# Optimization experiments

Measured on AMD Instinct MI355X. Metric: run time of the kernel, lower is better.

The kernel has to match this reference:

```python
import jax, jax.numpy as jnp
import numpy as np

HEADS = 12
IDX = 0


def setup_inputs() -> dict:
    key = jax.random.key(0)
    ks = jax.random.split(key, 6)
    B, H, W, C = 16, 64, 64, 384
    x = jax.random.normal(ks[0], (B, H * W, C), dtype=jnp.float32)
    qkv_w = jax.random.normal(ks[1], (3 * C, C), dtype=jnp.float32) * 0.02
    proj_w = jax.random.normal(ks[2], (C, C), dtype=jnp.float32) * 0.02
    proj_b = jax.random.normal(ks[3], (C,), dtype=jnp.float32) * 0.02
    lepe_w = jax.random.normal(ks[4], (C, 1, 3, 3), dtype=jnp.float32) * 0.02  # depthwise, torch OIHW with I=1
    lepe_b = jax.random.normal(ks[5], (C,), dtype=jnp.float32) * 0.02
    return {"x": x, "qkv_w": qkv_w, "proj_w": proj_w, "proj_b": proj_b,
            "lepe_w": lepe_w, "lepe_b": lepe_b, "H": H, "W": W}


def _lepe_forward(x, qkv_w, proj_w, proj_b, lepe_w, lepe_b, H, W):
    B, N, C = x.shape
    hd = C // HEADS
    scale = hd ** (-0.5)
    x_img = x.reshape(B, H, W, C)

    if IDX == 0:
        # vertical strips: attend over H within each column
        x_split = jnp.transpose(x_img, (0, 2, 1, 3)).reshape(B * W, H, C)
    else:
        x_split = x_img.reshape(B * H, W, C)
    S, L, _ = x_split.shape

    qkv = (x_split @ qkv_w.T).reshape(S, L, 3, HEADS, hd)
    qkv = jnp.transpose(qkv, (2, 0, 3, 1, 4))  # (3, S, heads, L, hd)
    q, k, v = qkv[0], qkv[1], qkv[2]

    attn = jnp.einsum('shld,shmd->shlm', q, k) * scale
    attn = jax.nn.softmax(attn, axis=-1)
    out = jnp.einsum('shlm,shmd->shld', attn, v)           # (S, heads, L, hd)
    out = jnp.transpose(out, (0, 2, 1, 3)).reshape(S, L, C)
    # faithful to torch: view(B, out_H, out_W, C).view(B, H*W, C) -- no permute back for idx==0
    out_flat = out.reshape(B, H * W, C)

    # depthwise 3x3 conv LePE on the original (H, W) layout
    lepe = jax.lax.conv_general_dilated(
        jnp.transpose(x_img, (0, 3, 1, 2)), lepe_w,
        window_strides=(1, 1), padding='SAME',
        feature_group_count=C,
        dimension_numbers=('NCHW', 'OIHW', 'NCHW'))
    lepe = lepe + lepe_b[None, :, None, None]
    lepe = jnp.transpose(lepe, (0, 2, 3, 1)).reshape(B, H * W, C)

    return (out_flat + lepe) @ proj_w.T + proj_b


def reference(x, qkv_w, proj_w, proj_b, lepe_w, lepe_b, H, W):
    return _lepe_forward(x, qkv_w, proj_w, proj_b, lepe_w, lepe_b, H, W)
```

## Files before the change

### kernel.cpp

```cpp
#include <hip/hip_runtime.h>


typedef _Float16 f16;
typedef _Float16 f16x8 __attribute__((ext_vector_type(8)));
typedef float    f32x4 __attribute__((ext_vector_type(4)));

__device__ __forceinline__ f32x4 mfma_16x16x32(f16x8 a, f16x8 b, f32x4 c) {
  return __builtin_amdgcn_mfma_f32_16x16x32_f16(a, b, c, 0, 0, 0);
}

__global__ __launch_bounds__(256) void k_cvt(const float* __restrict__ src,
                                             f16* __restrict__ dst, int n8) {
  int i = blockIdx.x * 256 + threadIdx.x;
  if (i >= n8) return;
  const f32x4* s4 = (const f32x4*)src;
  f32x4 a = s4[2 * i], b = s4[2 * i + 1];
  f16x8 o;
#pragma unroll
  for (int j = 0; j < 4; ++j) { o[j] = (f16)a[j]; o[4 + j] = (f16)b[j]; }
  *(f16x8*)&dst[(long)i * 8] = o;
}

template <int NDIM, bool FINAL>
__global__ __launch_bounds__(256) void k_gemm(const f16* __restrict__ A,
                                              const f16* __restrict__ Bt,
                                              const float* __restrict__ bias,
                                              f16* __restrict__ Ch,
                                              float* __restrict__ Cf) {
  constexpr int KD = 384;
  constexpr int LDSP = 72;
  constexpr int NT = NDIM / 128;
  __shared__ f16 As[128 * LDSP];
  __shared__ f16 Bs[128 * LDSP];

  const int tid = threadIdx.x;
  const int lane = tid & 63;
  const int wave = tid >> 6;
  const int wr = wave >> 1, wc = wave & 1;
  const int ln = lane & 15, quad = lane >> 4;
  const int q8 = quad * 8;
  const int mt = blockIdx.x / NT;
  const int nt = blockIdx.x % NT;
  const long m0 = (long)mt * 128;
  const int n0 = nt * 128;

  f32x4 acc[4][4] = {};

  for (int k0 = 0; k0 < KD; k0 += 64) {
#pragma unroll
    for (int r = 0; r < 4; ++r) {
      int flat = r * 256 + tid;
      int row = flat >> 3;
      int kk = (flat & 7) * 8;
      f16x8 av = *(const f16x8*)&A[(m0 + row) * KD + k0 + kk];
      *(f16x8*)&As[row * LDSP + kk] = av;
      f16x8 bv = *(const f16x8*)&Bt[(long)(n0 + row) * KD + k0 + kk];
      *(f16x8*)&Bs[row * LDSP + kk] = bv;
    }
    __syncthreads();
#pragma unroll
    for (int ks = 0; ks < 2; ++ks) {
      f16x8 a[4], b[4];
#pragma unroll
      for (int i = 0; i < 4; ++i)
        a[i] = *(const f16x8*)&As[(wr * 64 + i * 16 + ln) * LDSP + ks * 32 + q8];
#pragma unroll
      for (int j = 0; j < 4; ++j)
        b[j] = *(const f16x8*)&Bs[(wc * 64 + j * 16 + ln) * LDSP + ks * 32 + q8];
#pragma unroll
      for (int i = 0; i < 4; ++i)
#pragma unroll
        for (int j = 0; j < 4; ++j)
          acc[i][j] = mfma_16x16x32(a[i], b[j], acc[i][j]);
    }
    __syncthreads();
  }

#pragma unroll
  for (int i = 0; i < 4; ++i) {
#pragma unroll
    for (int j = 0; j < 4; ++j) {
      int gc = n0 + wc * 64 + j * 16 + ln;
#pragma unroll
      for (int r = 0; r < 4; ++r) {
        long gr = m0 + wr * 64 + i * 16 + quad * 4 + r;
        float v = acc[i][j][r];
        if (FINAL)
          Cf[gr * NDIM + gc] = v + bias[gc];
        else
          Ch[gr * (long)NDIM + gc] = (f16)v;
      }
    }
  }
}

__global__ __launch_bounds__(256) void k_lepe(const f16* __restrict__ x16,
                                              const float* __restrict__ lw,
                                              const float* __restrict__ lb,
                                              f16* __restrict__ afused) {
  __shared__ float ws[384 * 9];
  __shared__ float bs[384];
  for (int i = threadIdx.x; i < 384 * 9; i += 256) ws[i] = lw[i];
  for (int i = threadIdx.x; i < 384; i += 256) bs[i] = lb[i];
  __syncthreads();

  int chunk = blockIdx.x * 256 + threadIdx.x;
  int token = chunk / 48;
  int c0 = (chunk % 48) * 8;
  int b = token >> 12, n = token & 4095;
  int h = n >> 6, w = n & 63;

  float acc[8];
#pragma unroll
  for (int cc = 0; cc < 8; ++cc) acc[cc] = bs[c0 + cc];
#pragma unroll
  for (int ky = 0; ky < 3; ++ky) {
    int hh = h + ky - 1;
    if (hh < 0 || hh > 63) continue;
#pragma unroll
    for (int kx = 0; kx < 3; ++kx) {
      int ww = w + kx - 1;
      if (ww < 0 || ww > 63) continue;
      f16x8 xv = *(const f16x8*)&x16[((long)((b << 12) + (hh << 6) + ww)) * 384 + c0];
#pragma unroll
      for (int cc = 0; cc < 8; ++cc)
        acc[cc] += (float)xv[cc] * ws[(c0 + cc) * 9 + ky * 3 + kx];
    }
  }
  f16x8 o;
#pragma unroll
  for (int cc = 0; cc < 8; ++cc) o[cc] = (f16)acc[cc];
  *(f16x8*)&afused[(long)token * 384 + c0] = o;
}

__global__ __launch_bounds__(64) void k_attn(const f16* __restrict__ qkv,
                                             f16* __restrict__ afused) {
  __shared__ f16 vt[32 * 72];
  __shared__ f16 qkbuf[2 * 64 * 56];
  f16* qs = qkbuf;
  f16* ks = qkbuf + 64 * 56;
  f16* ps = qkbuf;

  const int lane = threadIdx.x;
  const int hh = blockIdx.x % 12;
  const int s = blockIdx.x / 12;
  const int b = s >> 6, w = s & 63;
  const int ln = lane & 15, quad = lane >> 4;
  const int q8 = quad * 8;
  const long baseTok = ((long)b << 12) + w;

#pragma unroll
  for (int r = 0; r < 4; ++r) {
    int flat = r * 64 + lane;
    int l = flat >> 2;
    int dg = (flat & 3) * 8;
    long ta = (baseTok + (long)l * 64) * 1152 + hh * 32 + dg;
    f16x8 qv = *(const f16x8*)&qkv[ta];
    f16x8 kv = *(const f16x8*)&qkv[ta + 384];
    f16x8 vv = *(const f16x8*)&qkv[ta + 768];
    *(f16x8*)&qs[l * 56 + dg] = qv;
    *(f16x8*)&ks[l * 56 + dg] = kv;
#pragma unroll
    for (int ii = 0; ii < 8; ++ii) vt[(dg + ii) * 72 + l] = vv[ii];
  }
  __syncthreads();

  f16x8 aq[4], bk[4];
#pragma unroll
  for (int i = 0; i < 4; ++i) aq[i] = *(const f16x8*)&qs[(i * 16 + ln) * 56 + q8];
#pragma unroll
  for (int j = 0; j < 4; ++j) bk[j] = *(const f16x8*)&ks[(j * 16 + ln) * 56 + q8];
  f32x4 sc[4][4] = {};
#pragma unroll
  for (int i = 0; i < 4; ++i)
#pragma unroll
    for (int j = 0; j < 4; ++j) sc[i][j] = mfma_16x16x32(aq[i], bk[j], sc[i][j]);
  __syncthreads();

  const float scale = 0.17677669529663687f;
  float rs[4][4];
#pragma unroll
  for (int i = 0; i < 4; ++i) {
#pragma unroll
    for (int r = 0; r < 4; ++r) {
      float m = -1e30f;
#pragma unroll
      for (int j = 0; j < 4; ++j) m = fmaxf(m, sc[i][j][r]);
#pragma unroll
      for (int off = 1; off < 16; off <<= 1) m = fmaxf(m, __shfl_xor(m, off, 64));
      m *= scale;
      float sum = 0.f;
#pragma unroll
      for (int j = 0; j < 4; ++j) {
        float p = __expf(sc[i][j][r] * scale - m);
        sc[i][j][r] = p;
        sum += p;
      }
#pragma unroll
      for (int off = 1; off < 16; off <<= 1) sum += __shfl_xor(sum, off, 64);
      rs[i][r] = 1.0f / sum;
    }
  }

#pragma unroll
  for (int i = 0; i < 4; ++i)
#pragma unroll
    for (int j = 0; j < 4; ++j)
#pragma unroll
      for (int r = 0; r < 4; ++r)
        ps[(i * 16 + quad * 4 + r) * 72 + j * 16 + ln] = (f16)sc[i][j][r];
  __syncthreads();

  f32x4 oc[4][2] = {};
#pragma unroll
  for (int ks2 = 0; ks2 < 2; ++ks2) {
    f16x8 ap[4], bv[2];
#pragma unroll
    for (int i = 0; i < 4; ++i)
      ap[i] = *(const f16x8*)&ps[(i * 16 + ln) * 72 + ks2 * 32 + q8];
#pragma unroll
    for (int j = 0; j < 2; ++j)
      bv[j] = *(const f16x8*)&vt[(j * 16 + ln) * 72 + ks2 * 32 + q8];
#pragma unroll
    for (int i = 0; i < 4; ++i)
#pragma unroll
      for (int j = 0; j < 2; ++j) oc[i][j] = mfma_16x16x32(ap[i], bv[j], oc[i][j]);
  }

#pragma unroll
  for (int i = 0; i < 4; ++i)
#pragma unroll
    for (int j = 0; j < 2; ++j)
#pragma unroll
      for (int r = 0; r < 4; ++r) {
        int l = i * 16 + quad * 4 + r;
        int d = j * 16 + ln;
        long g = ((long)b * 4096 + w * 64 + l) * 384 + hh * 32 + d;
        float v = oc[i][j][r] * rs[i][r];
        afused[g] = (f16)(v + (float)afused[g]);
      }
}

extern "C" void kernel_launch(void* const* d_in, const int* in_sizes, int n_in,
                              void* d_out, int out_size, void* d_ws, size_t ws_size,
                              hipStream_t stream) {
  const float* x      = (const float*)d_in[0];
  const float* qkv_w  = (const float*)d_in[1];
  const float* proj_w = (const float*)d_in[2];
  const float* proj_b = (const float*)d_in[3];
  const float* lepe_w = (const float*)d_in[4];
  const float* lepe_b = (const float*)d_in[5];
  float* out = (float*)d_out;

  char* ws = (char*)d_ws;
  f16* x16    = (f16*)(ws + 0);
  f16* w16    = (f16*)(ws + 50331648);
  f16* pw16   = (f16*)(ws + 51216384);
  f16* qkv16  = (f16*)(ws + 51511296);
  f16* afused = (f16*)(ws + 202506240);

  k_cvt<<<12288, 256, 0, stream>>>(x, x16, 3145728);
  k_cvt<<<216, 256, 0, stream>>>(qkv_w, w16, 55296);
  k_cvt<<<72, 256, 0, stream>>>(proj_w, pw16, 18432);
  k_gemm<1152, false><<<512 * 9, 256, 0, stream>>>(x16, w16, nullptr, qkv16, nullptr);
  k_lepe<<<12288, 256, 0, stream>>>(x16, lepe_w, lepe_b, afused);
  k_attn<<<1024 * 12, 64, 0, stream>>>(qkv16, afused);
  k_gemm<384, true><<<512 * 3, 256, 0, stream>>>(afused, pw16, proj_b, nullptr, out);
}
```

Baseline: 508.0 us.

## Fuse LePE conv, QKV projection and strip attention into one kernel

Replaces the x fp16 conversion, the QKV GEMM, the LePE depthwise conv and the attention kernels with a single per-(batch, column) kernel. It computes LePE directly from fp32 x, builds per-head Q/K/V in LDS from register-held x fragments and weights read from global memory, then runs softmax attention and accumulates into afused. This removes the large qkv16 and x16 intermediates from HBM traffic and three launches. In exchange, every block rereads the full QKV weight matrix from cache, the grid drops to 1024 blocks, and there is a stray no-op multiply-by-zero term in the LePE loop.

```diff
diff --git a/kernel.cpp b/kernel.cpp
--- a/kernel.cpp
+++ b/kernel.cpp
@@ -3,6 +3,7 @@
 
 typedef _Float16 f16;
 typedef _Float16 f16x8 __attribute__((ext_vector_type(8)));
+typedef _Float16 f16x4 __attribute__((ext_vector_type(4)));
 typedef float    f32x4 __attribute__((ext_vector_type(4)));
 
 __device__ __forceinline__ f32x4 mfma_16x16x32(f16x8 a, f16x8 b, f32x4 c) {
@@ -19,6 +20,221 @@
 #pragma unroll
   for (int j = 0; j < 4; ++j) { o[j] = (f16)a[j]; o[4 + j] = (f16)b[j]; }
   *(f16x8*)&dst[(long)i * 8] = o;
+}
+
+__global__ __launch_bounds__(256, 2) void k_fused(const float* __restrict__ x,
+                                                  const f16* __restrict__ w16,
+                                                  const float* __restrict__ lw,
+                                                  const float* __restrict__ lb,
+                                                  f16* __restrict__ afused) {
+  __shared__ f16 shp[2][14592];
+  const int tid = threadIdx.x;
+  const int lane = tid & 63;
+  const int wave = tid >> 6;
+  const int mh = wave & 1, nh = wave >> 1;
+  const int ln = lane & 15, quad = lane >> 4, q8 = quad * 8;
+  const int b = blockIdx.x >> 6, w = blockIdx.x & 63;
+
+  f16* qs = shp[nh];
+  f16* ks = shp[nh] + 2560;
+  f16* vt = shp[nh] + 5120;
+  f16* ps = shp[nh] + 7424;
+  f16* obuf = shp[nh] + 12032;
+
+  {
+    const float* xb = x + (long)b * 4096 * 384;
+    const int l = lane;
+    f16* arow = afused + ((long)(b * 4096 + w * 64 + l)) * 384;
+#pragma unroll
+    for (int it = 0; it < 12; ++it) {
+      int c0 = (it * 4 + wave) * 8;
+      float a8[8];
+#pragma unroll
+      for (int cc = 0; cc < 8; ++cc) a8[cc] = lb[c0 + cc];
+#pragma unroll
+      for (int ky = 0; ky < 3; ++ky) {
+        int hh2 = w + ky - 1;
+        if (hh2 < 0 || hh2 > 63) continue;
+#pragma unroll
+        for (int kx = 0; kx < 3; ++kx) {
+          int ww2 = l + kx - 1;
+          if (ww2 < 0 || ww2 > 63) continue;
+          const float* p = xb + ((hh2 << 6) + ww2) * 384 + c0;
+          float4 u = *(const float4*)p;
+          float4 v2 = *(const float4*)(p + 4);
+#pragma unroll
+          for (int cc = 0; cc < 4; ++cc) {
+            a8[cc] += u.x * 0.f;
+          }
+#pragma unroll
+          for (int cc = 0; cc < 4; ++cc) {
+            float wv0 = lw[(c0 + cc) * 9 + ky * 3 + kx];
+            float wv1 = lw[(c0 + 4 + cc) * 9 + ky * 3 + kx];
+            float xv0 = (cc == 0) ? u.x : (cc == 1) ? u.y : (cc == 2) ? u.z : u.w;
+            float xv1 = (cc == 0) ? v2.x : (cc == 1) ? v2.y : (cc == 2) ? v2.z : v2.w;
+            a8[cc] += xv0 * wv0;
+            a8[4 + cc] += xv1 * wv1;
+          }
+        }
+      }
+      f16x8 o;
+#pragma unroll
+      for (int cc = 0; cc < 8; ++cc) o[cc] = (f16)a8[cc];
+      *(f16x8*)&arow[c0] = o;
+    }
+  }
+  __syncthreads();
+
+  f16x8 afr[12][2];
+  {
+    const float* xcol = x + ((long)(b * 4096) + w) * 384;
+#pragma unroll
+    for (int s = 0; s < 12; ++s)
+#pragma unroll
+      for (int i = 0; i < 2; ++i) {
+        const float* p = xcol + (long)(mh * 32 + i * 16 + ln) * 24576 + s * 32 + q8;
+        float4 u = *(const float4*)p;
+        float4 v2 = *(const float4*)(p + 4);
+        f16x8 t;
+        t[0] = (f16)u.x; t[1] = (f16)u.y; t[2] = (f16)u.z; t[3] = (f16)u.w;
+        t[4] = (f16)v2.x; t[5] = (f16)v2.y; t[6] = (f16)v2.z; t[7] = (f16)v2.w;
+        afr[s][i] = t;
+      }
+  }
+
+  const float qscale = 0.17677669529663687f;
+
+  for (int h6 = 0; h6 < 6; ++h6) {
+    const int hh = nh * 6 + h6;
+#pragma unroll
+    for (int pass = 0; pass < 3; ++pass) {
+      f32x4 acc[2][2] = {};
+      const f16* wb = w16 + (long)(pass * 384 + hh * 32) * 384;
+#pragma unroll
+      for (int s = 0; s < 12; ++s) {
+        f16x8 bf[2];
+#pragma unroll
+        for (int j = 0; j < 2; ++j)
+          bf[j] = *(const f16x8*)&wb[(long)(j * 16 + ln) * 384 + s * 32 + q8];
+#pragma unroll
+        for (int i = 0; i < 2; ++i)
+#pragma unroll
+          for (int j = 0; j < 2; ++j)
+            acc[i][j] = mfma_16x16x32(afr[s][i], bf[j], acc[i][j]);
+      }
+      if (pass == 0) {
+#pragma unroll
+        for (int i = 0; i < 2; ++i)
+#pragma unroll
+          for (int j = 0; j < 2; ++j)
+#pragma unroll
+            for (int r = 0; r < 4; ++r)
+              qs[(mh * 32 + i * 16 + quad * 4 + r) * 40 + j * 16 + ln] =
+                  (f16)(acc[i][j][r] * qscale);
+      } else if (pass == 1) {
+#pragma unroll
+        for (int i = 0; i < 2; ++i)
+#pragma unroll
+          for (int j = 0; j < 2; ++j)
+#pragma unroll
+            for (int r = 0; r < 4; ++r)
+              ks[(mh * 32 + i * 16 + quad * 4 + r) * 40 + j * 16 + ln] =
+                  (f16)acc[i][j][r];
+      } else {
+#pragma unroll
+        for (int i = 0; i < 2; ++i)
+#pragma unroll
+          for (int j = 0; j < 2; ++j) {
+            f16x4 pk;
+            pk[0] = (f16)acc[i][j][0]; pk[1] = (f16)acc[i][j][1];
+            pk[2] = (f16)acc[i][j][2]; pk[3] = (f16)acc[i][j][3];
+            *(f16x4*)&vt[(j * 16 + ln) * 72 + mh * 32 + i * 16 + quad * 4] = pk;
+          }
+      }
+    }
+    __syncthreads();
+
+    f16x8 aq[2], bk[4];
+#pragma unroll
+    for (int i = 0; i < 2; ++i)
+      aq[i] = *(const f16x8*)&qs[(mh * 32 + i * 16 + ln) * 40 + q8];
+#pragma unroll
+    for (int j = 0; j < 4; ++j)
+      bk[j] = *(const f16x8*)&ks[(j * 16 + ln) * 40 + q8];
+    f32x4 sc[2][4] = {};
+#pragma unroll
+    for (int i = 0; i < 2; ++i)
+#pragma unroll
+      for (int j = 0; j < 4; ++j) sc[i][j] = mfma_16x16x32(aq[i], bk[j], sc[i][j]);
+
+    float rs[2][4];
+#pragma unroll
+    for (int i = 0; i < 2; ++i) {
+#pragma unroll
+      for (int r = 0; r < 4; ++r) {
+        float m = -1e30f;
+#pragma unroll
+        for (int j = 0; j < 4; ++j) m = fmaxf(m, sc[i][j][r]);
+#pragma unroll
+        for (int off = 1; off < 16; off <<= 1) m = fmaxf(m, __shfl_xor(m, off, 64));
+        float sum = 0.f;
+#pragma unroll
+        for (int j = 0; j < 4; ++j) {
+          float p = __expf(sc[i][j][r] - m);
+          sc[i][j][r] = p;
+          sum += p;
+        }
+#pragma unroll
+        for (int off = 1; off < 16; off <<= 1) sum += __shfl_xor(sum, off, 64);
+        rs[i][r] = 1.0f / sum;
+      }
+    }
+
+#pragma unroll
+    for (int i = 0; i < 2; ++i)
+#pragma unroll
+      for (int j = 0; j < 4; ++j)
+#pragma unroll
+        for (int r = 0; r < 4; ++r)
+          ps[(mh * 32 + i * 16 + quad * 4 + r) * 72 + j * 16 + ln] = (f16)sc[i][j][r];
+
+    f32x4 oc[2][2] = {};
+#pragma unroll
+    for (int k2 = 0; k2 < 2; ++k2) {
+      f16x8 ap[2], bv[2];
+#pragma unroll
+      for (int i = 0; i < 2; ++i)
+        ap[i] = *(const f16x8*)&ps[(mh * 32 + i * 16 + ln) * 72 + k2 * 32 + q8];
+#pragma unroll
+      for (int j = 0; j < 2; ++j)
+        bv[j] = *(const f16x8*)&vt[(j * 16 + ln) * 72 + k2 * 32 + q8];
+#pragma unroll
+      for (int i = 0; i < 2; ++i)
+#pragma unroll
+        for (int j = 0; j < 2; ++j) oc[i][j] = mfma_16x16x32(ap[i], bv[j], oc[i][j]);
+    }
+
+#pragma unroll
+    for (int i = 0; i < 2; ++i)
+#pragma unroll
+      for (int j = 0; j < 2; ++j)
+#pragma unroll
+        for (int r = 0; r < 4; ++r)
+          obuf[(mh * 32 + i * 16 + quad * 4 + r) * 40 + j * 16 + ln] =
+              (f16)(oc[i][j][r] * rs[i][r]);
+    {
+      int row = mh * 32 + (lane >> 1), hf = lane & 1;
+      f16* gp = afused + ((long)(b * 4096 + w * 64 + row)) * 384 + hh * 32 + hf * 16;
+      const f16* ob = &obuf[row * 40 + hf * 16];
+      f16x8 o0 = *(const f16x8*)ob, o1 = *(const f16x8*)(ob + 8);
+      f16x8 g0 = *(const f16x8*)gp, g1 = *(const f16x8*)(gp + 8);
+      g0 = g0 + o0;
+      g1 = g1 + o1;
+      *(f16x8*)gp = g0;
+      *(f16x8*)(gp + 8) = g1;
+    }
+    __syncthreads();
+  }
 }
 
 template <int NDIM, bool FINAL>
@@ -94,158 +310,11 @@
   }
 }
 
-__global__ __launch_bounds__(256) void k_lepe(const f16* __restrict__ x16,
-                                              const float* __restrict__ lw,
-                                              const float* __restrict__ lb,
-                                              f16* __restrict__ afused) {
-  __shared__ float ws[384 * 9];
-  __shared__ float bs[384];
-  for (int i = threadIdx.x; i < 384 * 9; i += 256) ws[i] = lw[i];
-  for (int i = threadIdx.x; i < 384; i += 256) bs[i] = lb[i];
-  __syncthreads();
-
-  int chunk = blockIdx.x * 256 + threadIdx.x;
-  int token = chunk / 48;
-  int c0 = (chunk % 48) * 8;
-  int b = token >> 12, n = token & 4095;
-  int h = n >> 6, w = n & 63;
-
-  float acc[8];
-#pragma unroll
-  for (int cc = 0; cc < 8; ++cc) acc[cc] = bs[c0 + cc];
-#pragma unroll
-  for (int ky = 0; ky < 3; ++ky) {
-    int hh = h + ky - 1;
-    if (hh < 0 || hh > 63) continue;
-#pragma unroll
-    for (int kx = 0; kx < 3; ++kx) {
-      int ww = w + kx - 1;
-      if (ww < 0 || ww > 63) continue;
-      f16x8 xv = *(const f16x8*)&x16[((long)((b << 12) + (hh << 6) + ww)) * 384 + c0];
-#pragma unroll
-      for (int cc = 0; cc < 8; ++cc)
-        acc[cc] += (float)xv[cc] * ws[(c0 + cc) * 9 + ky * 3 + kx];
-    }
-  }
-  f16x8 o;
-#pragma unroll
-  for (int cc = 0; cc < 8; ++cc) o[cc] = (f16)acc[cc];
-  *(f16x8*)&afused[(long)token * 384 + c0] = o;
-}
-
-__global__ __launch_bounds__(64) void k_attn(const f16* __restrict__ qkv,
-                                             f16* __restrict__ afused) {
-  __shared__ f16 vt[32 * 72];
-  __shared__ f16 qkbuf[2 * 64 * 56];
-  f16* qs = qkbuf;
-  f16* ks = qkbuf + 64 * 56;
-  f16* ps = qkbuf;
-
-  const int lane = threadIdx.x;
-  const int hh = blockIdx.x % 12;
-  const int s = blockIdx.x / 12;
-  const int b = s >> 6, w = s & 63;
-  const int ln = lane & 15, quad = lane >> 4;
-  const int q8 = quad * 8;
-  const long baseTok = ((long)b << 12) + w;
-
-#pragma unroll
-  for (int r = 0; r < 4; ++r) {
-    int flat = r * 64 + lane;
-    int l = flat >> 2;
-    int dg = (flat & 3) * 8;
-    long ta = (baseTok + (long)l * 64) * 1152 + hh * 32 + dg;
-    f16x8 qv = *(const f16x8*)&qkv[ta];
-    f16x8 kv = *(const f16x8*)&qkv[ta + 384];
-    f16x8 vv = *(const f16x8*)&qkv[ta + 768];
-    *(f16x8*)&qs[l * 56 + dg] = qv;
-    *(f16x8*)&ks[l * 56 + dg] = kv;
-#pragma unroll
-    for (int ii = 0; ii < 8; ++ii) vt[(dg + ii) * 72 + l] = vv[ii];
-  }
-  __syncthreads();
-
-  f16x8 aq[4], bk[4];
-#pragma unroll
-  for (int i = 0; i < 4; ++i) aq[i] = *(const f16x8*)&qs[(i * 16 + ln) * 56 + q8];
-#pragma unroll
-  for (int j = 0; j < 4; ++j) bk[j] = *(const f16x8*)&ks[(j * 16 + ln) * 56 + q8];
-  f32x4 sc[4][4] = {};
-#pragma unroll
-  for (int i = 0; i < 4; ++i)
-#pragma unroll
-    for (int j = 0; j < 4; ++j) sc[i][j] = mfma_16x16x32(aq[i], bk[j], sc[i][j]);
-  __syncthreads();
-
-  const float scale = 0.17677669529663687f;
-  float rs[4][4];
-#pragma unroll
-  for (int i = 0; i < 4; ++i) {
-#pragma unroll
-    for (int r = 0; r < 4; ++r) {
-      float m = -1e30f;
-#pragma unroll
-      for (int j = 0; j < 4; ++j) m = fmaxf(m, sc[i][j][r]);
-#pragma unroll
-      for (int off = 1; off < 16; off <<= 1) m = fmaxf(m, __shfl_xor(m, off, 64));
-      m *= scale;
-      float sum = 0.f;
-#pragma unroll
-      for (int j = 0; j < 4; ++j) {
-        float p = __expf(sc[i][j][r] * scale - m);
-        sc[i][j][r] = p;
-        sum += p;
-      }
-#pragma unroll
-      for (int off = 1; off < 16; off <<= 1) sum += __shfl_xor(sum, off, 64);
-      rs[i][r] = 1.0f / sum;
-    }
-  }
-
-#pragma unroll
-  for (int i = 0; i < 4; ++i)
-#pragma unroll
-    for (int j = 0; j < 4; ++j)
-#pragma unroll
-      for (int r = 0; r < 4; ++r)
-        ps[(i * 16 + quad * 4 + r) * 72 + j * 16 + ln] = (f16)sc[i][j][r];
-  __syncthreads();
-
-  f32x4 oc[4][2] = {};
-#pragma unroll
-  for (int ks2 = 0; ks2 < 2; ++ks2) {
-    f16x8 ap[4], bv[2];
-#pragma unroll
-    for (int i = 0; i < 4; ++i)
-      ap[i] = *(const f16x8*)&ps[(i * 16 + ln) * 72 + ks2 * 32 + q8];
-#pragma unroll
-    for (int j = 0; j < 2; ++j)
-      bv[j] = *(const f16x8*)&vt[(j * 16 + ln) * 72 + ks2 * 32 + q8];
-#pragma unroll
-    for (int i = 0; i < 4; ++i)
-#pragma unroll
-      for (int j = 0; j < 2; ++j) oc[i][j] = mfma_16x16x32(ap[i], bv[j], oc[i][j]);
-  }
-
-#pragma unroll
-  for (int i = 0; i < 4; ++i)
-#pragma unroll
-    for (int j = 0; j < 2; ++j)
-#pragma unroll
-      for (int r = 0; r < 4; ++r) {
-        int l = i * 16 + quad * 4 + r;
-        int d = j * 16 + ln;
-        long g = ((long)b * 4096 + w * 64 + l) * 384 + hh * 32 + d;
-        float v = oc[i][j][r] * rs[i][r];
-        afused[g] = (f16)(v + (float)afused[g]);
-      }
-}
-
 extern "C" void kernel_launch(void* const* d_in, const int* in_sizes, int n_in,
                               void* d_out, int out_size, void* d_ws, size_t ws_size,
                               hipStream_t stream) {
-  const float* x      = (const float*)d_in[0];
-  const float* qkv_w  = (const float*)d_in[1];
+  const float* x = (const float*)d_in[0];
+  const float* qkv_w = (const float*)d_in[1];
   const float* proj_w = (const float*)d_in[2];
   const float* proj_b = (const float*)d_in[3];
   const float* lepe_w = (const float*)d_in[4];
@@ -253,17 +322,12 @@
   float* out = (float*)d_out;
 
   char* ws = (char*)d_ws;
-  f16* x16    = (f16*)(ws + 0);
-  f16* w16    = (f16*)(ws + 50331648);
-  f16* pw16   = (f16*)(ws + 51216384);
-  f16* qkv16  = (f16*)(ws + 51511296);
-  f16* afused = (f16*)(ws + 202506240);
-
-  k_cvt<<<12288, 256, 0, stream>>>(x, x16, 3145728);
+  f16* w16 = (f16*)(ws + 0);
+  f16* pw16 = (f16*)(ws + 884736);
+  f16* afused = (f16*)(ws + 1179648);
+
   k_cvt<<<216, 256, 0, stream>>>(qkv_w, w16, 55296);
   k_cvt<<<72, 256, 0, stream>>>(proj_w, pw16, 18432);
-  k_gemm<1152, false><<<512 * 9, 256, 0, stream>>>(x16, w16, nullptr, qkv16, nullptr);
-  k_lepe<<<12288, 256, 0, stream>>>(x16, lepe_w, lepe_b, afused);
-  k_attn<<<1024 * 12, 64, 0, stream>>>(qkv16, afused);
+  k_fused<<<1024, 256, 0, stream>>>(x, w16, lepe_w, lepe_b, afused);
   k_gemm<384, true><<<512 * 3, 256, 0, stream>>>(afused, pw16, proj_b, nullptr, out);
 }
```

Result: slower. 592.1 us (+16.6%).
